# Kernel optimization log

Hardware: AMD Instinct MI355X
Metric: run time of the kernel (lower is better)

The kernel has to match this reference:

```python
import jax, jax.numpy as jnp
import numpy as np

T, B, E, H, F = 1024, 2, 1024, 16, 8
D = E // H
R = 2 * T - 1  # relative positions T-1 .. -(T-1)


def setup_inputs() -> dict:
    key = jax.random.key(0)
    ks = jax.random.split(key, 11)
    std = float(np.sqrt(2.0 / (E + E)))
    return {
        "input": jax.random.normal(ks[0], (T, B, E), jnp.float32),
        "pos": jax.random.normal(ks[1], (R, B, E), jnp.float32),
        "factor": jax.random.normal(ks[2], (F,), jnp.float32),
        "in_proj_weight": jax.random.normal(ks[3], (3 * E * E, F), jnp.float32) * std,
        "pos_proj_weight": jax.random.normal(ks[4], (E * E, F), jnp.float32) * std,
        "out_proj_weight": jax.random.normal(ks[5], (E * E, F), jnp.float32) * std,
        "in_proj_bias": jax.random.normal(ks[6], (3 * E, F), jnp.float32) * 0.02,
        "pos_proj_bias": jax.random.normal(ks[7], (E, F), jnp.float32) * 0.02,
        "out_proj_bias": jax.random.normal(ks[8], (E, F), jnp.float32) * 0.02,
        "r_w_bias": jax.random.normal(ks[9], (E, F), jnp.float32) * 0.02,
        "r_r_bias": jax.random.normal(ks[10], (E, F), jnp.float32) * 0.02,
    }


def _rel_shift(x):
    # x: [BH, T, R] -> out[b, i, j] = x[b, i, j + (T-1) - i]
    bh, q, r = x.shape
    zp = jnp.zeros((bh, q, 1), x.dtype)
    xp = jnp.concatenate([zp, x], axis=2).reshape(bh, r + 1, q)
    return xp[:, 1:, :].reshape(bh, q, r)


def reference(input, pos, factor, in_proj_weight, pos_proj_weight, out_proj_weight,
              in_proj_bias, pos_proj_bias, out_proj_bias, r_w_bias, r_r_bias):
    # hypernetwork: generate effective weights from factor vector (torch.mv)
    W_in = (in_proj_weight @ factor).reshape(3 * E, E)
    W_pos = (pos_proj_weight @ factor).reshape(E, E)
    W_out = (out_proj_weight @ factor).reshape(E, E)
    b_in = in_proj_bias @ factor
    b_pos = pos_proj_bias @ factor
    b_out = out_proj_bias @ factor
    rw = (r_w_bias @ factor).reshape(H, D)  # content bias
    rr = (r_r_bias @ factor).reshape(H, D)  # position bias

    qkv = input @ W_in.T + b_in                      # [T, B, 3E]
    q, k, v = jnp.split(qkv, 3, axis=-1)
    q = q.reshape(T, B, H, D)
    k = k.reshape(T, B, H, D)
    v = v.reshape(T, B, H, D)
    r = (pos @ W_pos.T + b_pos).reshape(R, B, H, D)  # [R, B, H, D]

    scale = 1.0 / np.sqrt(D)
    # AC: content-content + content bias term
    AC = jnp.einsum('ibhd,jbhd->bhij', q + rw, k)    # [B, H, T, T]
    # BD: content-position + position bias term, then relative shift
    BD = jnp.einsum('ibhd,rbhd->bhir', q + rr, r)    # [B, H, T, R]
    BD = _rel_shift(BD.reshape(B * H, T, R))[:, :, :T].reshape(B, H, T, T)

    attn = jax.nn.softmax((AC + BD) * scale, axis=-1)  # [B, H, T, T]
    out = jnp.einsum('bhij,jbhd->ibhd', attn, v).reshape(T, B, E)
    out = out @ W_out.T + b_out                       # [T, B, E]
    return out
```

## Files before the change

kernel.cpp:

```cpp
#include <hip/hip_runtime.h>


typedef _Float16 h16;
typedef _Float16 h16x8 __attribute__((ext_vector_type(8)));
typedef _Float16 h16x4 __attribute__((ext_vector_type(4)));
typedef float f32x4 __attribute__((ext_vector_type(4)));

static __device__ __forceinline__ f32x4 mfma16(h16x8 a, h16x8 b, f32x4 c) {
  return __builtin_amdgcn_mfma_f32_16x16x32_f16(a, b, c, 0, 0, 0);
}

static __device__ __forceinline__ void gload16(const void* g, void* l) {
  __builtin_amdgcn_global_load_lds((const __attribute__((address_space(1))) void*)g,
                                   (__attribute__((address_space(3))) void*)l, 16, 0, 0);
}

__global__ __launch_bounds__(256) void hypernet_kernel(
    const float* __restrict__ fac,
    const float* __restrict__ w_in, const float* __restrict__ w_pos,
    const float* __restrict__ w_out, const float* __restrict__ b_in_w,
    const float* __restrict__ b_pos_w, const float* __restrict__ b_out_w,
    const float* __restrict__ rw_w, const float* __restrict__ rr_w,
    h16* __restrict__ Win, h16* __restrict__ Wpos, h16* __restrict__ Wout,
    float* __restrict__ bin, float* __restrict__ bpos, float* __restrict__ bout,
    float* __restrict__ rw, float* __restrict__ rr, h16* __restrict__ rb)
{
  int idx = blockIdx.x * 256 + threadIdx.x;
  float f0=fac[0],f1=fac[1],f2=fac[2],f3=fac[3],f4=fac[4],f5=fac[5],f6=fac[6],f7=fac[7];
#define DOT8(p) ((p)[0]*f0+(p)[1]*f1+(p)[2]*f2+(p)[3]*f3+(p)[4]*f4+(p)[5]*f5+(p)[6]*f6+(p)[7]*f7)
  if (idx < 3145728) { const float* p = w_in  + (size_t)idx*8; Win[idx]  = (h16)DOT8(p); return; }
  idx -= 3145728;
  if (idx < 1048576) { const float* p = w_pos + (size_t)idx*8; Wpos[idx] = (h16)DOT8(p); return; }
  idx -= 1048576;
  if (idx < 1048576) { const float* p = w_out + (size_t)idx*8; Wout[idx] = (h16)DOT8(p); return; }
  idx -= 1048576;
  if (idx < 3072) { bin[idx]  = DOT8(b_in_w  + (size_t)idx*8); return; }
  idx -= 3072;
  if (idx < 1024) { bpos[idx] = DOT8(b_pos_w + (size_t)idx*8); return; }
  idx -= 1024;
  if (idx < 1024) { bout[idx] = DOT8(b_out_w + (size_t)idx*8); return; }
  idx -= 1024;
  if (idx < 1024) { rw[idx]   = DOT8(rw_w    + (size_t)idx*8); return; }
  idx -= 1024;
  if (idx < 1024) { rr[idx]   = DOT8(rr_w    + (size_t)idx*8); return; }
  idx -= 1024;
  if (idx < 2048) {
    rb[(((size_t)(idx >> 6)) << 17) + 2047*64 + (idx & 63)] = (h16)0.f;
  }
#undef DOT8
}

__global__ __launch_bounds__(256) void cvt_f2h_kernel(
    const float* __restrict__ in, h16* __restrict__ out, int n4)
{
  int i = blockIdx.x * 256 + threadIdx.x;
  if (i >= n4) return;
  float4 v = reinterpret_cast<const float4*>(in)[i];
  h16x4 o = { (h16)v.x, (h16)v.y, (h16)v.z, (h16)v.w };
  reinterpret_cast<h16x4*>(out)[i] = o;
}

template <int MODE>
__global__ __launch_bounds__(256) void gemm_lds_kernel(
    const h16* __restrict__ A, const h16* __restrict__ Bw,
    const float* __restrict__ bias, int M, int N, int K,
    float* __restrict__ Cout,
    const float* __restrict__ rwv, const float* __restrict__ rrv,
    h16* __restrict__ o0, h16* __restrict__ o1,
    h16* __restrict__ o2, h16* __restrict__ o3)
{
  __shared__ __align__(16) h16 a_sm[128*64];
  __shared__ __align__(16) h16 b_sm[128*64];
  const int tid = threadIdx.x, lane = tid & 63, wave = tid >> 6;
  const int quad = lane >> 4, t16 = lane & 15;
  const int wm = wave >> 1, wn = wave & 1;
  const int m0 = blockIdx.y * 128, n0 = blockIdx.x * 128;
  const int lrow = lane >> 3, lcol = (lane & 7) * 8;

  f32x4 acc[4][4];
#pragma unroll
  for (int i = 0; i < 4; ++i)
#pragma unroll
    for (int j = 0; j < 4; ++j) acc[i][j] = (f32x4){0.f,0.f,0.f,0.f};

  for (int k0 = 0; k0 < K; k0 += 64) {
    __syncthreads();
#pragma unroll
    for (int s = 0; s < 4; ++s) {
      int rbase = wave*32 + s*8;
      gload16(A  + (size_t)(m0 + rbase + lrow)*K + k0 + lcol, a_sm + rbase*64);
      gload16(Bw + (size_t)(n0 + rbase + lrow)*K + k0 + lcol, b_sm + rbase*64);
    }
    __syncthreads();
#pragma unroll
    for (int kc = 0; kc < 2; ++kc) {
      h16x8 af[4], bfr[4];
#pragma unroll
      for (int i = 0; i < 4; ++i) {
        af[i]  = *reinterpret_cast<const h16x8*>(a_sm + (wm*64 + i*16 + t16)*64 + kc*32 + quad*8);
        bfr[i] = *reinterpret_cast<const h16x8*>(b_sm + (wn*64 + i*16 + t16)*64 + kc*32 + quad*8);
      }
#pragma unroll
      for (int i = 0; i < 4; ++i)
#pragma unroll
        for (int j = 0; j < 4; ++j)
          acc[i][j] = mfma16(af[i], bfr[j], acc[i][j]);
    }
  }

#pragma unroll
  for (int i = 0; i < 4; ++i) {
    int mb = m0 + wm*64 + i*16 + quad*4;
#pragma unroll
    for (int j = 0; j < 4; ++j) {
      int n = n0 + wn*64 + j*16 + t16;
      float bv = bias[n];
      if (MODE == 2) {
#pragma unroll
        for (int r = 0; r < 4; ++r)
          Cout[(size_t)(mb + r)*N + n] = acc[i][j][r] + bv;
      } else if (MODE == 0) {
        int nn = n & 1023, sec = n >> 10, hh = nn >> 6, d = nn & 63;
        float rwb = rwv[nn], rrb = rrv[nn];
#pragma unroll
        for (int r = 0; r < 4; ++r) {
          int m = mb + r, t = m >> 1, b = m & 1;
          size_t off = ((size_t)((b << 4) + hh) << 16) + (t << 6) + d;
          float v = acc[i][j][r] + bv;
          if (sec == 0)      { o0[off] = (h16)(v + rwb); o1[off] = (h16)(v + rrb); }
          else if (sec == 1) { o2[off] = (h16)v; }
          else               { o3[off] = (h16)v; }
        }
      } else {
        int hh = n >> 6, d = n & 63;
#pragma unroll
        for (int r = 0; r < 4; ++r) {
          int m = mb + r;
          if (m < M) {
            int rel = m >> 1, b = m & 1;
            o0[(((size_t)((b << 4) + hh)) << 17) + (rel << 6) + d] = (h16)(acc[i][j][r] + bv);
          }
        }
      }
    }
  }
}

__global__ __launch_bounds__(256) void transpose_v_kernel(
    const h16* __restrict__ vb, h16* __restrict__ vbt)
{
  __shared__ h16 tile[64*72];
  const int bh = blockIdx.y, t0 = blockIdx.x * 64;
  const int r = threadIdx.x >> 3, c = (threadIdx.x & 7) * 8;
  const h16* src = vb + ((size_t)bh << 16) + (size_t)(t0 + r)*64 + c;
  *reinterpret_cast<h16x8*>(tile + r*72 + c)        = *reinterpret_cast<const h16x8*>(src);
  *reinterpret_cast<h16x8*>(tile + (r + 32)*72 + c) = *reinterpret_cast<const h16x8*>(src + 32*64);
  __syncthreads();
  h16x8 o0, o1;
#pragma unroll
  for (int e = 0; e < 8; ++e) {
    o0[e] = tile[(c + e)*72 + r];
    o1[e] = tile[(c + e)*72 + r + 32];
  }
  h16* dst = vbt + ((size_t)bh << 16) + (size_t)r*1024 + t0 + c;
  *reinterpret_cast<h16x8*>(dst)            = o0;
  *reinterpret_cast<h16x8*>(dst + 32*1024)  = o1;
}

__global__ __launch_bounds__(256) void flash_kernel(
    const h16* __restrict__ qrw, const h16* __restrict__ qrr,
    const h16* __restrict__ kb, const h16* __restrict__ vbt,
    const h16* __restrict__ rb,
    float* __restrict__ o_part, float* __restrict__ ml_part)
{
  __shared__ __align__(16) h16 k_sm[64*64];
  __shared__ __align__(16) h16 vt_sm[64*64];
  __shared__ __align__(16) h16 r_sm[128*64];

  const int tid = threadIdx.x, lane = tid & 63, wave = tid >> 6;
  const int quad = lane >> 4, t16 = lane & 15;
  const int bh = blockIdx.y, i0 = blockIdx.x * 64, jh = blockIdx.z;
  const size_t base  = (size_t)bh << 16;
  const size_t rbase = (size_t)bh << 17;
  const int iw = i0 + wave * 16;
  const int lrow = lane >> 3, lcol = (lane & 7) * 8;

  h16x8 a_rw[2], a_rr[2];
  {
    const h16* p = qrw + base + (size_t)(iw + t16)*64 + quad*8;
    a_rw[0] = *reinterpret_cast<const h16x8*>(p);
    a_rw[1] = *reinterpret_cast<const h16x8*>(p + 32);
    const h16* p2 = qrr + base + (size_t)(iw + t16)*64 + quad*8;
    a_rr[0] = *reinterpret_cast<const h16x8*>(p2);
    a_rr[1] = *reinterpret_cast<const h16x8*>(p2 + 32);
  }

  f32x4 o_acc[4];
#pragma unroll
  for (int dc = 0; dc < 4; ++dc) o_acc[dc] = (f32x4){0.f,0.f,0.f,0.f};
  float m_run[4] = {-1e30f,-1e30f,-1e30f,-1e30f};
  float l_run[4] = {0.f,0.f,0.f,0.f};

  h16* bdw = r_sm + wave * (16*84);
  const int cb0 = 3 - wave;

  for (int j0 = jh*512; j0 < jh*512 + 512; j0 += 64) {
    __syncthreads();
    {
#pragma unroll
      for (int s = 0; s < 2; ++s) {
        int row = wave*16 + s*8;
        gload16(kb  + base + (size_t)(j0 + row + lrow)*64 + lcol, k_sm  + row*64);
        gload16(vbt + base + (size_t)(row + lrow)*1024 + j0 + lcol, vt_sm + row*64);
      }
      const int rel0 = j0 - i0 + 960;
#pragma unroll
      for (int s = 0; s < 4; ++s) {
        int row = wave*32 + s*8;
        gload16(rb + rbase + (size_t)(rel0 + row + lrow)*64 + lcol, r_sm + row*64);
      }
    }
    __syncthreads();

    f32x4 s_ac[4];
#pragma unroll
    for (int c = 0; c < 4; ++c) {
      s_ac[c] = (f32x4){0.f,0.f,0.f,0.f};
#pragma unroll
      for (int kc = 0; kc < 2; ++kc) {
        h16x8 b = *reinterpret_cast<const h16x8*>(k_sm + (c*16 + t16)*64 + kc*32 + quad*8);
        s_ac[c] = mfma16(a_rw[kc], b, s_ac[c]);
      }
    }
    f32x4 s_bd[5];
#pragma unroll
    for (int u = 0; u < 5; ++u) {
      s_bd[u] = (f32x4){0.f,0.f,0.f,0.f};
#pragma unroll
      for (int kc = 0; kc < 2; ++kc) {
        h16x8 b = *reinterpret_cast<const h16x8*>(r_sm + ((cb0+u)*16 + t16)*64 + kc*32 + quad*8);
        s_bd[u] = mfma16(a_rr[kc], b, s_bd[u]);
      }
    }
    __syncthreads();

#pragma unroll
    for (int u = 0; u < 5; ++u)
#pragma unroll
      for (int r = 0; r < 4; ++r)
        bdw[(quad*4 + r)*84 + u*16 + t16] = (h16)s_bd[u][r];

    float sv[4][4];
#pragma unroll
    for (int c = 0; c < 4; ++c)
#pragma unroll
      for (int r = 0; r < 4; ++r) {
        int il = quad*4 + r;
        float bdv = (float)bdw[il*84 + c*16 + t16 + 15 - il];
        sv[c][r] = (s_ac[c][r] + bdv) * 0.125f;
      }

    float alpha[4];
#pragma unroll
    for (int r = 0; r < 4; ++r) {
      float v = fmaxf(fmaxf(sv[0][r], sv[1][r]), fmaxf(sv[2][r], sv[3][r]));
#pragma unroll
      for (int off = 1; off < 16; off <<= 1) v = fmaxf(v, __shfl_xor(v, off, 64));
      float mn = fmaxf(m_run[r], v);
      alpha[r] = __expf(m_run[r] - mn);
      m_run[r] = mn;
    }
#pragma unroll
    for (int r = 0; r < 4; ++r) {
      float s0 = 0.f;
#pragma unroll
      for (int c = 0; c < 4; ++c) {
        float p = __expf(sv[c][r] - m_run[r]);
        sv[c][r] = p; s0 += p;
      }
#pragma unroll
      for (int off = 1; off < 16; off <<= 1) s0 += __shfl_xor(s0, off, 64);
      l_run[r] = l_run[r]*alpha[r] + s0;
    }
#pragma unroll
    for (int dc = 0; dc < 4; ++dc) {
      f32x4 t = o_acc[dc];
#pragma unroll
      for (int r = 0; r < 4; ++r) t[r] *= alpha[r];
      o_acc[dc] = t;
    }
    h16* pw = bdw;
#pragma unroll
    for (int c = 0; c < 4; ++c)
#pragma unroll
      for (int r = 0; r < 4; ++r)
        pw[(quad*4 + r)*72 + c*16 + t16] = (h16)sv[c][r];

    h16x8 ap0 = *reinterpret_cast<const h16x8*>(pw + t16*72 + quad*8);
    h16x8 ap1 = *reinterpret_cast<const h16x8*>(pw + t16*72 + 32 + quad*8);
#pragma unroll
    for (int dc = 0; dc < 4; ++dc) {
      h16x8 bv0 = *reinterpret_cast<const h16x8*>(vt_sm + (dc*16 + t16)*64 + quad*8);
      h16x8 bv1 = *reinterpret_cast<const h16x8*>(vt_sm + (dc*16 + t16)*64 + 32 + quad*8);
      o_acc[dc] = mfma16(ap0, bv0, o_acc[dc]);
      o_acc[dc] = mfma16(ap1, bv1, o_acc[dc]);
    }
  }

  const size_t obase = ((size_t)jh*32 + bh) * 1024 * 64;
#pragma unroll
  for (int r = 0; r < 4; ++r) {
    int i = iw + quad*4 + r;
#pragma unroll
    for (int dc = 0; dc < 4; ++dc)
      o_part[obase + (size_t)i*64 + dc*16 + t16] = o_acc[dc][r];
    if (t16 == 0) {
      size_t mo = (((size_t)jh*32 + bh)*1024 + i)*2;
      ml_part[mo]     = m_run[r];
      ml_part[mo + 1] = l_run[r];
    }
  }
}

__global__ __launch_bounds__(256) void combine_kernel(
    const float* __restrict__ o_part, const float* __restrict__ ml_part,
    h16* __restrict__ attn_h)
{
  int gid = blockIdx.x * 256 + threadIdx.x;
  int row = gid >> 4;
  int d4 = (gid & 15) * 4;
  float m1 = ml_part[row*2], l1 = ml_part[row*2 + 1];
  float m2 = ml_part[65536 + row*2], l2 = ml_part[65536 + row*2 + 1];
  float M = fmaxf(m1, m2);
  float e1 = __expf(m1 - M), e2 = __expf(m2 - M);
  float inv = 1.f / (e1*l1 + e2*l2);
  float4 O1 = *reinterpret_cast<const float4*>(o_part + (size_t)row*64 + d4);
  float4 O2 = *reinterpret_cast<const float4*>(o_part + 2097152 + (size_t)row*64 + d4);
  int bh = row >> 10, i = row & 1023, b = bh >> 4, h = bh & 15;
  h16x4 o = { (h16)((e1*O1.x + e2*O2.x) * inv), (h16)((e1*O1.y + e2*O2.y) * inv),
              (h16)((e1*O1.z + e2*O2.z) * inv), (h16)((e1*O1.w + e2*O2.w) * inv) };
  *reinterpret_cast<h16x4*>(attn_h + ((size_t)(i*2 + b))*1024 + h*64 + d4) = o;
}

extern "C" void kernel_launch(void* const* d_in, const int* in_sizes, int n_in,
                              void* d_out, int out_size, void* d_ws, size_t ws_size,
                              hipStream_t stream)
{
  const float* input  = (const float*)d_in[0];
  const float* pos    = (const float*)d_in[1];
  const float* fac    = (const float*)d_in[2];
  const float* w_in   = (const float*)d_in[3];
  const float* w_pos  = (const float*)d_in[4];
  const float* w_out  = (const float*)d_in[5];
  const float* bin_w  = (const float*)d_in[6];
  const float* bpos_w = (const float*)d_in[7];
  const float* bout_w = (const float*)d_in[8];
  const float* rw_w   = (const float*)d_in[9];
  const float* rr_w   = (const float*)d_in[10];
  float* out = (float*)d_out;
  (void)in_sizes; (void)n_in; (void)out_size; (void)ws_size;

  char* w = (char*)d_ws;
  auto take = [&](size_t bytes) { char* p = w; w += bytes; return p; };
  h16*   Win    = (h16*)take(3145728ull*2);
  h16*   Wpos   = (h16*)take(1048576ull*2);
  h16*   Wout   = (h16*)take(1048576ull*2);
  float* bin    = (float*)take(3072*4);
  float* bpos   = (float*)take(1024*4);
  float* bout   = (float*)take(1024*4);
  float* rw     = (float*)take(1024*4);
  float* rr     = (float*)take(1024*4);
  h16*   in_h   = (h16*)take(2097152ull*2);
  h16*   pos_h  = (h16*)take(4192256ull*2);
  h16*   qrwb   = (h16*)take(2097152ull*2);
  h16*   qrrb   = (h16*)take(2097152ull*2);
  h16*   kb     = (h16*)take(2097152ull*2);
  h16*   vb     = (h16*)take(2097152ull*2);
  h16*   vbt    = (h16*)take(2097152ull*2);
  h16*   rb     = (h16*)take(4194304ull*2);
  float* o_part = (float*)take(4194304ull*4);
  float* ml     = (float*)take(131072ull*4);
  h16*   attn_h = (h16*)take(2097152ull*2);

  hypernet_kernel<<<20516, 256, 0, stream>>>(fac, w_in, w_pos, w_out, bin_w, bpos_w, bout_w,
                                             rw_w, rr_w, Win, Wpos, Wout, bin, bpos, bout,
                                             rw, rr, rb);
  cvt_f2h_kernel<<<2048, 256, 0, stream>>>(input, in_h, 524288);
  cvt_f2h_kernel<<<4094, 256, 0, stream>>>(pos, pos_h, 1048064);
  gemm_lds_kernel<0><<<dim3(24, 16), 256, 0, stream>>>(in_h, Win, bin, 2048, 3072, 1024,
                                                       nullptr, rw, rr, qrwb, qrrb, kb, vb);
  gemm_lds_kernel<1><<<dim3(8, 32), 256, 0, stream>>>(pos_h, Wpos, bpos, 4094, 1024, 1024,
                                                      nullptr, nullptr, nullptr, rb, nullptr, nullptr, nullptr);
  transpose_v_kernel<<<dim3(16, 32), 256, 0, stream>>>(vb, vbt);
  flash_kernel<<<dim3(16, 32, 2), 256, 0, stream>>>(qrwb, qrrb, kb, vbt, rb, o_part, ml);
  combine_kernel<<<2048, 256, 0, stream>>>(o_part, ml, attn_h);
  gemm_lds_kernel<2><<<dim3(8, 16), 256, 0, stream>>>(attn_h, Wout, bout, 2048, 1024, 1024,
                                                      out, nullptr, nullptr, nullptr, nullptr, nullptr, nullptr);
}
```

Measured before the change: 379.0 us.

## Swizzle LDS layouts, split flash KV into 4 parts, fuse conversions into hypernet

Applies an XOR swizzle to the 16-byte granules loaded into LDS in both the GEMM and flash kernels, to avoid bank conflicts on the MFMA fragment reads. Splits the flash attention key range into 4 chunks instead of 2, doubling the block count, and widens the combine kernel to merge 4 partials. Defers the row-sum shuffle reduction to the end of the flash kernel. Folds the two fp32-to-fp16 conversion kernels into the hypernet kernel to save launches. The cost is larger partial-output buffers and more combine traffic.

```diff
diff --git a/kernel.cpp b/kernel.cpp
--- a/kernel.cpp
+++ b/kernel.cpp
@@ -9,7 +9,6 @@
 static __device__ __forceinline__ f32x4 mfma16(h16x8 a, h16x8 b, f32x4 c) {
   return __builtin_amdgcn_mfma_f32_16x16x32_f16(a, b, c, 0, 0, 0);
 }
-
 static __device__ __forceinline__ void gload16(const void* g, void* l) {
   __builtin_amdgcn_global_load_lds((const __attribute__((address_space(1))) void*)g,
                                    (__attribute__((address_space(3))) void*)l, 16, 0, 0);
@@ -23,7 +22,9 @@
     const float* __restrict__ rw_w, const float* __restrict__ rr_w,
     h16* __restrict__ Win, h16* __restrict__ Wpos, h16* __restrict__ Wout,
     float* __restrict__ bin, float* __restrict__ bpos, float* __restrict__ bout,
-    float* __restrict__ rw, float* __restrict__ rr, h16* __restrict__ rb)
+    float* __restrict__ rw, float* __restrict__ rr, h16* __restrict__ rb,
+    const float* __restrict__ input, h16* __restrict__ in_h,
+    const float* __restrict__ pos, h16* __restrict__ pos_h)
 {
   int idx = blockIdx.x * 256 + threadIdx.x;
   float f0=fac[0],f1=fac[1],f2=fac[2],f3=fac[3],f4=fac[4],f5=fac[5],f6=fac[6],f7=fac[7];
@@ -44,20 +45,21 @@
   idx -= 1024;
   if (idx < 1024) { rr[idx]   = DOT8(rr_w    + (size_t)idx*8); return; }
   idx -= 1024;
-  if (idx < 2048) {
-    rb[(((size_t)(idx >> 6)) << 17) + 2047*64 + (idx & 63)] = (h16)0.f;
+  if (idx < 2048) { rb[(((size_t)(idx >> 6)) << 17) + 2047*64 + (idx & 63)] = (h16)0.f; return; }
+  idx -= 2048;
+  if (idx < 524288) {
+    float4 v = reinterpret_cast<const float4*>(input)[idx];
+    h16x4 o = { (h16)v.x, (h16)v.y, (h16)v.z, (h16)v.w };
+    reinterpret_cast<h16x4*>(in_h)[idx] = o;
+    return;
+  }
+  idx -= 524288;
+  if (idx < 1048064) {
+    float4 v = reinterpret_cast<const float4*>(pos)[idx];
+    h16x4 o = { (h16)v.x, (h16)v.y, (h16)v.z, (h16)v.w };
+    reinterpret_cast<h16x4*>(pos_h)[idx] = o;
   }
 #undef DOT8
-}
-
-__global__ __launch_bounds__(256) void cvt_f2h_kernel(
-    const float* __restrict__ in, h16* __restrict__ out, int n4)
-{
-  int i = blockIdx.x * 256 + threadIdx.x;
-  if (i >= n4) return;
-  float4 v = reinterpret_cast<const float4*>(in)[i];
-  h16x4 o = { (h16)v.x, (h16)v.y, (h16)v.z, (h16)v.w };
-  reinterpret_cast<h16x4*>(out)[i] = o;
 }
 
 template <int MODE>
@@ -75,7 +77,10 @@
   const int quad = lane >> 4, t16 = lane & 15;
   const int wm = wave >> 1, wn = wave & 1;
   const int m0 = blockIdx.y * 128, n0 = blockIdx.x * 128;
-  const int lrow = lane >> 3, lcol = (lane & 7) * 8;
+  const int lrow = lane >> 3, lgran = lane & 7;
+  const int gsw = (lgran ^ lrow) * 8;
+  const int xg0 = (quad ^ (t16 & 7)) * 8;
+  const int xg1 = xg0 ^ 32;
 
   f32x4 acc[4][4];
 #pragma unroll
@@ -88,17 +93,18 @@
 #pragma unroll
     for (int s = 0; s < 4; ++s) {
       int rbase = wave*32 + s*8;
-      gload16(A  + (size_t)(m0 + rbase + lrow)*K + k0 + lcol, a_sm + rbase*64);
-      gload16(Bw + (size_t)(n0 + rbase + lrow)*K + k0 + lcol, b_sm + rbase*64);
+      gload16(A  + (size_t)(m0 + rbase + lrow)*K + k0 + gsw, a_sm + rbase*64);
+      gload16(Bw + (size_t)(n0 + rbase + lrow)*K + k0 + gsw, b_sm + rbase*64);
     }
     __syncthreads();
 #pragma unroll
     for (int kc = 0; kc < 2; ++kc) {
+      const int xg = kc ? xg1 : xg0;
       h16x8 af[4], bfr[4];
 #pragma unroll
       for (int i = 0; i < 4; ++i) {
-        af[i]  = *reinterpret_cast<const h16x8*>(a_sm + (wm*64 + i*16 + t16)*64 + kc*32 + quad*8);
-        bfr[i] = *reinterpret_cast<const h16x8*>(b_sm + (wn*64 + i*16 + t16)*64 + kc*32 + quad*8);
+        af[i]  = *reinterpret_cast<const h16x8*>(a_sm + (wm*64 + i*16 + t16)*64 + xg);
+        bfr[i] = *reinterpret_cast<const h16x8*>(b_sm + (wn*64 + i*16 + t16)*64 + xg);
       }
 #pragma unroll
       for (int i = 0; i < 4; ++i)
@@ -183,7 +189,10 @@
   const size_t base  = (size_t)bh << 16;
   const size_t rbase = (size_t)bh << 17;
   const int iw = i0 + wave * 16;
-  const int lrow = lane >> 3, lcol = (lane & 7) * 8;
+  const int lrow = lane >> 3, lgran = lane & 7;
+  const int gsw = (lgran ^ lrow) * 8;
+  const int xg0 = (quad ^ (t16 & 7)) * 8;
+  const int xg1 = xg0 ^ 32;
 
   h16x8 a_rw[2], a_rr[2];
   {
@@ -204,20 +213,20 @@
   h16* bdw = r_sm + wave * (16*84);
   const int cb0 = 3 - wave;
 
-  for (int j0 = jh*512; j0 < jh*512 + 512; j0 += 64) {
+  for (int j0 = jh*256; j0 < jh*256 + 256; j0 += 64) {
     __syncthreads();
     {
 #pragma unroll
       for (int s = 0; s < 2; ++s) {
         int row = wave*16 + s*8;
-        gload16(kb  + base + (size_t)(j0 + row + lrow)*64 + lcol, k_sm  + row*64);
-        gload16(vbt + base + (size_t)(row + lrow)*1024 + j0 + lcol, vt_sm + row*64);
+        gload16(kb  + base + (size_t)(j0 + row + lrow)*64 + gsw, k_sm  + row*64);
+        gload16(vbt + base + (size_t)(row + lrow)*1024 + j0 + gsw, vt_sm + row*64);
       }
       const int rel0 = j0 - i0 + 960;
 #pragma unroll
       for (int s = 0; s < 4; ++s) {
         int row = wave*32 + s*8;
-        gload16(rb + rbase + (size_t)(rel0 + row + lrow)*64 + lcol, r_sm + row*64);
+        gload16(rb + rbase + (size_t)(rel0 + row + lrow)*64 + gsw, r_sm + row*64);
       }
     }
     __syncthreads();
@@ -226,21 +235,15 @@
 #pragma unroll
     for (int c = 0; c < 4; ++c) {
       s_ac[c] = (f32x4){0.f,0.f,0.f,0.f};
-#pragma unroll
-      for (int kc = 0; kc < 2; ++kc) {
-        h16x8 b = *reinterpret_cast<const h16x8*>(k_sm + (c*16 + t16)*64 + kc*32 + quad*8);
-        s_ac[c] = mfma16(a_rw[kc], b, s_ac[c]);
-      }
+      s_ac[c] = mfma16(a_rw[0], *reinterpret_cast<const h16x8*>(k_sm + (c*16 + t16)*64 + xg0), s_ac[c]);
+      s_ac[c] = mfma16(a_rw[1], *reinterpret_cast<const h16x8*>(k_sm + (c*16 + t16)*64 + xg1), s_ac[c]);
     }
     f32x4 s_bd[5];
 #pragma unroll
     for (int u = 0; u < 5; ++u) {
       s_bd[u] = (f32x4){0.f,0.f,0.f,0.f};
-#pragma unroll
-      for (int kc = 0; kc < 2; ++kc) {
-        h16x8 b = *reinterpret_cast<const h16x8*>(r_sm + ((cb0+u)*16 + t16)*64 + kc*32 + quad*8);
-        s_bd[u] = mfma16(a_rr[kc], b, s_bd[u]);
-      }
+      s_bd[u] = mfma16(a_rr[0], *reinterpret_cast<const h16x8*>(r_sm + ((cb0+u)*16 + t16)*64 + xg0), s_bd[u]);
+      s_bd[u] = mfma16(a_rr[1], *reinterpret_cast<const h16x8*>(r_sm + ((cb0+u)*16 + t16)*64 + xg1), s_bd[u]);
     }
     __syncthreads();
 
@@ -278,8 +281,6 @@
         float p = __expf(sv[c][r] - m_run[r]);
         sv[c][r] = p; s0 += p;
       }
-#pragma unroll
-      for (int off = 1; off < 16; off <<= 1) s0 += __shfl_xor(s0, off, 64);
       l_run[r] = l_run[r]*alpha[r] + s0;
     }
 #pragma unroll
@@ -300,13 +301,20 @@
     h16x8 ap1 = *reinterpret_cast<const h16x8*>(pw + t16*72 + 32 + quad*8);
 #pragma unroll
     for (int dc = 0; dc < 4; ++dc) {
-      h16x8 bv0 = *reinterpret_cast<const h16x8*>(vt_sm + (dc*16 + t16)*64 + quad*8);
-      h16x8 bv1 = *reinterpret_cast<const h16x8*>(vt_sm + (dc*16 + t16)*64 + 32 + quad*8);
+      h16x8 bv0 = *reinterpret_cast<const h16x8*>(vt_sm + (dc*16 + t16)*64 + xg0);
+      h16x8 bv1 = *reinterpret_cast<const h16x8*>(vt_sm + (dc*16 + t16)*64 + xg1);
       o_acc[dc] = mfma16(ap0, bv0, o_acc[dc]);
       o_acc[dc] = mfma16(ap1, bv1, o_acc[dc]);
     }
   }
 
+#pragma unroll
+  for (int r = 0; r < 4; ++r) {
+    float l = l_run[r];
+#pragma unroll
+    for (int off = 1; off < 16; off <<= 1) l += __shfl_xor(l, off, 64);
+    l_run[r] = l;
+  }
   const size_t obase = ((size_t)jh*32 + bh) * 1024 * 64;
 #pragma unroll
   for (int r = 0; r < 4; ++r) {
@@ -329,16 +337,25 @@
   int gid = blockIdx.x * 256 + threadIdx.x;
   int row = gid >> 4;
   int d4 = (gid & 15) * 4;
-  float m1 = ml_part[row*2], l1 = ml_part[row*2 + 1];
-  float m2 = ml_part[65536 + row*2], l2 = ml_part[65536 + row*2 + 1];
-  float M = fmaxf(m1, m2);
-  float e1 = __expf(m1 - M), e2 = __expf(m2 - M);
-  float inv = 1.f / (e1*l1 + e2*l2);
-  float4 O1 = *reinterpret_cast<const float4*>(o_part + (size_t)row*64 + d4);
-  float4 O2 = *reinterpret_cast<const float4*>(o_part + 2097152 + (size_t)row*64 + d4);
+  float m[4], l[4];
+#pragma unroll
+  for (int p = 0; p < 4; ++p) {
+    m[p] = ml_part[p*65536 + row*2];
+    l[p] = ml_part[p*65536 + row*2 + 1];
+  }
+  float M = fmaxf(fmaxf(m[0], m[1]), fmaxf(m[2], m[3]));
+  float e[4], den = 0.f;
+#pragma unroll
+  for (int p = 0; p < 4; ++p) { e[p] = __expf(m[p] - M); den += e[p]*l[p]; }
+  float inv = 1.f / den;
+  float4 acc = {0.f,0.f,0.f,0.f};
+#pragma unroll
+  for (int p = 0; p < 4; ++p) {
+    float4 O = *reinterpret_cast<const float4*>(o_part + (size_t)p*2097152 + (size_t)row*64 + d4);
+    acc.x += e[p]*O.x; acc.y += e[p]*O.y; acc.z += e[p]*O.z; acc.w += e[p]*O.w;
+  }
   int bh = row >> 10, i = row & 1023, b = bh >> 4, h = bh & 15;
-  h16x4 o = { (h16)((e1*O1.x + e2*O2.x) * inv), (h16)((e1*O1.y + e2*O2.y) * inv),
-              (h16)((e1*O1.z + e2*O2.z) * inv), (h16)((e1*O1.w + e2*O2.w) * inv) };
+  h16x4 o = { (h16)(acc.x*inv), (h16)(acc.y*inv), (h16)(acc.z*inv), (h16)(acc.w*inv) };
   *reinterpret_cast<h16x4*>(attn_h + ((size_t)(i*2 + b))*1024 + h*64 + d4) = o;
 }
 
@@ -378,21 +395,19 @@
   h16*   vb     = (h16*)take(2097152ull*2);
   h16*   vbt    = (h16*)take(2097152ull*2);
   h16*   rb     = (h16*)take(4194304ull*2);
-  float* o_part = (float*)take(4194304ull*4);
-  float* ml     = (float*)take(131072ull*4);
+  float* o_part = (float*)take(4ull*2097152ull*4);
+  float* ml     = (float*)take(4ull*65536ull*4);
   h16*   attn_h = (h16*)take(2097152ull*2);
 
-  hypernet_kernel<<<20516, 256, 0, stream>>>(fac, w_in, w_pos, w_out, bin_w, bpos_w, bout_w,
+  hypernet_kernel<<<26658, 256, 0, stream>>>(fac, w_in, w_pos, w_out, bin_w, bpos_w, bout_w,
                                              rw_w, rr_w, Win, Wpos, Wout, bin, bpos, bout,
-                                             rw, rr, rb);
-  cvt_f2h_kernel<<<2048, 256, 0, stream>>>(input, in_h, 524288);
-  cvt_f2h_kernel<<<4094, 256, 0, stream>>>(pos, pos_h, 1048064);
+                                             rw, rr, rb, input, in_h, pos, pos_h);
   gemm_lds_kernel<0><<<dim3(24, 16), 256, 0, stream>>>(in_h, Win, bin, 2048, 3072, 1024,
                                                        nullptr, rw, rr, qrwb, qrrb, kb, vb);
   gemm_lds_kernel<1><<<dim3(8, 32), 256, 0, stream>>>(pos_h, Wpos, bpos, 4094, 1024, 1024,
                                                       nullptr, nullptr, nullptr, rb, nullptr, nullptr, nullptr);
   transpose_v_kernel<<<dim3(16, 32), 256, 0, stream>>>(vb, vbt);
-  flash_kernel<<<dim3(16, 32, 2), 256, 0, stream>>>(qrwb, qrrb, kb, vbt, rb, o_part, ml);
+  flash_kernel<<<dim3(16, 32, 4), 256, 0, stream>>>(qrwb, qrrb, kb, vbt, rb, o_part, ml);
   combine_kernel<<<2048, 256, 0, stream>>>(o_part, ml, attn_h);
   gemm_lds_kernel<2><<<dim3(8, 16), 256, 0, stream>>>(attn_h, Wout, bout, 2048, 1024, 1024,
                                                       out, nullptr, nullptr, nullptr, nullptr, nullptr, nullptr);
```

Result: faster. 356.7 us (-5.9%).
